# Optimization experiments

Hardware: AMD Instinct MI355X
Metric: run time of the kernel (lower is better)

## Reference

```python
import jax, jax.numpy as jnp
import numpy as np

LOSS_WEIGHT = 1.0

def setup_inputs() -> dict:
    key = jax.random.key(0)
    k1, k2 = jax.random.split(key)
    point_set_1 = jax.random.normal(k1, (8, 4096, 2), dtype=jnp.float32)
    point_set_2 = jax.random.normal(k2, (8, 4096, 2), dtype=jnp.float32)
    return {"point_set_1": point_set_1, "point_set_2": point_set_2}

def reference(point_set_1, point_set_2):
    # Pairwise L2 distances: C[n, i, j] = ||x[n,i] - y[n,j]||_2  -> (N, P1, P2)
    diff = point_set_1[:, :, None, :] - point_set_2[:, None, :, :]
    C = jnp.sqrt(jnp.sum(diff * diff, axis=-1))
    d1 = jnp.min(C, axis=-1).mean(axis=-1)  # x -> nearest y
    d2 = jnp.min(C, axis=-2).mean(axis=-1)  # y -> nearest x
    dist = (d1 + d2) / 2.0                   # (N,)
    return dist * LOSS_WEIGHT
```

## Files before the change

kernel.cpp:

```cpp
#include <hip/hip_runtime.h>
#include <hip/hip_bf16.h>
#include <math.h>


#define B 8
#define N 4096
#define NJ 16
#define NI 2
#define S1B 256
#define TX 8
#define JC (N / NJ)


__global__ __launch_bounds__(256) void chamfer_init(unsigned* __restrict__ mind2) {
  mind2[blockIdx.x * 256 + threadIdx.x] = 0x7F800000u;
}

__global__ __launch_bounds__(S1B) void chamfer_stage1(
    const float2* __restrict__ P1, const float2* __restrict__ P2,
    unsigned* __restrict__ mind2) {
  __shared__ float4 yb[JC];

  int b = blockIdx.x;
  int c = b & (NJ - 1);
  int itile = (b >> 4) & (NI - 1);
  int n = (b >> 5) & (B - 1);
  int dir = b >> 8;

  const float2* __restrict__ Q = dir ? P2 : P1;
  const float2* __restrict__ D = dir ? P1 : P2;

  const float2* dbase = D + n * N + c * JC;
  for (int t = threadIdx.x; t < JC; t += S1B) {
    float2 p = dbase[t];
    yb[t] = make_float4(-2.f * p.x, -2.f * p.y,
                        fmaf(p.x, p.x, p.y * p.y), 0.f);
  }
  __syncthreads();

  float qx[TX], qy[TX], qq[TX], m[TX];
  const float2* qbase = Q + n * N + itile * (S1B * TX) + threadIdx.x;
#pragma unroll
  for (int k = 0; k < TX; ++k) {
    float2 q = qbase[k * S1B];
    qx[k] = q.x; qy[k] = q.y;
    qq[k] = fmaf(q.x, q.x, q.y * q.y);
    m[k] = INFINITY;
  }

#pragma unroll 4
  for (int j = 0; j < JC; ++j) {
    float4 y = yb[j];
#pragma unroll
    for (int k = 0; k < TX; ++k) {
      float t = fmaf(qx[k], y.x, fmaf(qy[k], y.y, y.z));
      m[k] = fminf(m[k], t);
    }
  }

  unsigned* __restrict__ dst =
      mind2 + (dir * B + n) * N + itile * (S1B * TX) + threadIdx.x;
#pragma unroll
  for (int k = 0; k < TX; ++k) {
    float d2 = fmaxf(m[k] + qq[k], 0.f);
    atomicMin(dst + k * S1B, __float_as_uint(d2));
  }
}

__global__ __launch_bounds__(256) void chamfer_stage2(
    const unsigned* __restrict__ mind2, float* __restrict__ out) {
  int n = blockIdx.x;
  float acc = 0.f;
#pragma unroll
  for (int dir = 0; dir < 2; ++dir) {
    const unsigned* __restrict__ p = mind2 + (dir * B + n) * N;
#pragma unroll
    for (int s = 0; s < N / 256; ++s)
      acc += sqrtf(__uint_as_float(p[threadIdx.x + s * 256]));
  }
  __shared__ float red[256];
  red[threadIdx.x] = acc;
  __syncthreads();
  for (int s = 128; s > 0; s >>= 1) {
    if (threadIdx.x < s) red[threadIdx.x] += red[threadIdx.x + s];
    __syncthreads();
  }
  if (threadIdx.x == 0) out[n] = red[0] * (0.5f / (float)N);
}

extern "C" void kernel_launch(void* const* d_in, const int* in_sizes, int n_in,
                              void* d_out, int out_size, void* d_ws, size_t ws_size,
                              hipStream_t stream) {
  const float2* P1 = (const float2*)d_in[0];
  const float2* P2 = (const float2*)d_in[1];
  float* out = (float*)d_out;
  unsigned* mind2 = (unsigned*)d_ws;

  chamfer_init<<<dim3(2 * B * N / 256), 256, 0, stream>>>(mind2);
  chamfer_stage1<<<dim3(2 * B * NI * NJ), S1B, 0, stream>>>(P1, P2, mind2);
  chamfer_stage2<<<dim3(B), 256, 0, stream>>>(mind2, out);
}
```

Measured before the change: 30.23 us.

## Use v_min3 in inner loop, vectorize init, split final reduction across blocks

Three changes. The init kernel now writes 16-byte vectors with a quarter of the blocks and also zeroes per-batch counters. The stage-1 inner loop processes two y points per step and combines the mins with a single v_min3_f32 via inline asm, cutting VALU min instructions. Stage 2 grows from 8 blocks to 64, with a last-block-done atomic counter pattern doing the final sum, which adds fences and atomics but spreads the memory reads over more CUs.

```diff
diff --git a/kernel.cpp b/kernel.cpp
--- a/kernel.cpp
+++ b/kernel.cpp
@@ -12,8 +12,13 @@
 #define JC (N / NJ)
 
 
-__global__ __launch_bounds__(256) void chamfer_init(unsigned* __restrict__ mind2) {
-  mind2[blockIdx.x * 256 + threadIdx.x] = 0x7F800000u;
+typedef unsigned uint4v __attribute__((ext_vector_type(4)));
+
+__global__ __launch_bounds__(256) void chamfer_init(unsigned* __restrict__ mind2,
+                                                    unsigned* __restrict__ cnt) {
+  uint4v v = {0x7F800000u, 0x7F800000u, 0x7F800000u, 0x7F800000u};
+  ((uint4v*)mind2)[blockIdx.x * 256 + threadIdx.x] = v;
+  if (blockIdx.x == 0 && threadIdx.x < B) cnt[threadIdx.x] = 0u;
 }
 
 __global__ __launch_bounds__(S1B) void chamfer_stage1(
@@ -48,13 +53,15 @@
     m[k] = INFINITY;
   }
 
-#pragma unroll 4
-  for (int j = 0; j < JC; ++j) {
-    float4 y = yb[j];
+#pragma unroll 2
+  for (int jp = 0; jp < JC; jp += 2) {
+    float4 y0 = yb[jp];
+    float4 y1 = yb[jp + 1];
 #pragma unroll
     for (int k = 0; k < TX; ++k) {
-      float t = fmaf(qx[k], y.x, fmaf(qy[k], y.y, y.z));
-      m[k] = fminf(m[k], t);
+      float t0 = fmaf(qx[k], y0.x, fmaf(qy[k], y0.y, y0.z));
+      float t1 = fmaf(qx[k], y1.x, fmaf(qy[k], y1.y, y1.z));
+      asm("v_min3_f32 %0, %0, %1, %2" : "+v"(m[k]) : "v"(t0), "v"(t1));
     }
   }
 
@@ -68,16 +75,18 @@
 }
 
 __global__ __launch_bounds__(256) void chamfer_stage2(
-    const unsigned* __restrict__ mind2, float* __restrict__ out) {
-  int n = blockIdx.x;
-  float acc = 0.f;
-#pragma unroll
-  for (int dir = 0; dir < 2; ++dir) {
-    const unsigned* __restrict__ p = mind2 + (dir * B + n) * N;
-#pragma unroll
-    for (int s = 0; s < N / 256; ++s)
-      acc += sqrtf(__uint_as_float(p[threadIdx.x + s * 256]));
-  }
+    const unsigned* __restrict__ mind2, float* __restrict__ bs,
+    unsigned* __restrict__ cnt, float* __restrict__ out) {
+  int bid = blockIdx.x;
+  int n = bid >> 3, g = bid & 7;
+  int i = g * 512 + threadIdx.x;
+
+  float acc =
+      sqrtf(__uint_as_float(mind2[(0 * B + n) * N + i])) +
+      sqrtf(__uint_as_float(mind2[(0 * B + n) * N + i + 256])) +
+      sqrtf(__uint_as_float(mind2[(1 * B + n) * N + i])) +
+      sqrtf(__uint_as_float(mind2[(1 * B + n) * N + i + 256]));
+
   __shared__ float red[256];
   red[threadIdx.x] = acc;
   __syncthreads();
@@ -85,7 +94,22 @@
     if (threadIdx.x < s) red[threadIdx.x] += red[threadIdx.x + s];
     __syncthreads();
   }
-  if (threadIdx.x == 0) out[n] = red[0] * (0.5f / (float)N);
+
+  if (threadIdx.x == 0) {
+    bs[bid] = red[0];
+    __threadfence();
+    unsigned old = atomicAdd(&cnt[n], 1u);
+    if (old == 7u) {
+      __threadfence();
+      float v = 0.f;
+#pragma unroll
+      for (int gg = 0; gg < 8; ++gg)
+        v += __uint_as_float(__hip_atomic_load(
+            (const unsigned*)&bs[n * 8 + gg],
+            __ATOMIC_RELAXED, __HIP_MEMORY_SCOPE_AGENT));
+      out[n] = v * (0.5f / (float)N);
+    }
+  }
 }
 
 extern "C" void kernel_launch(void* const* d_in, const int* in_sizes, int n_in,
@@ -94,9 +118,12 @@
   const float2* P1 = (const float2*)d_in[0];
   const float2* P2 = (const float2*)d_in[1];
   float* out = (float*)d_out;
+
   unsigned* mind2 = (unsigned*)d_ws;
+  float* bs = (float*)(mind2 + 2 * B * N);
+  unsigned* cnt = (unsigned*)(bs + 64);
 
-  chamfer_init<<<dim3(2 * B * N / 256), 256, 0, stream>>>(mind2);
+  chamfer_init<<<dim3(2 * B * N / 1024), 256, 0, stream>>>(mind2, cnt);
   chamfer_stage1<<<dim3(2 * B * NI * NJ), S1B, 0, stream>>>(P1, P2, mind2);
-  chamfer_stage2<<<dim3(B), 256, 0, stream>>>(mind2, out);
+  chamfer_stage2<<<dim3(64), 256, 0, stream>>>(mind2, bs, cnt, out);
 }
```

After: 31.70 us. +4.9%, slower.
